# Kernel tuning notes

Hardware: AMD Instinct MI355X
Metric: run time of the kernel (lower is better)

Reference implementation:

```python
import jax, jax.numpy as jnp
import numpy as np

N_HEADS = 8
N_POINTS = 4


def _bilinear_sample(vl, g, Hl, Wl):
    # vl: [B, nH, Hl*Wl, hd] level values; g: [B, Q, nH, P, 2] sampling locs in [0,1] (x, y)
    # Emulates torch grid_sample(mode='bilinear', padding_mode='zeros', align_corners=False)
    B, Q, nH, P, _ = g.shape
    hd = vl.shape[-1]
    x = g[..., 0] * Wl - 0.5
    y = g[..., 1] * Hl - 0.5
    x0f = jnp.floor(x)
    y0f = jnp.floor(y)
    x0 = x0f.astype(jnp.int32)
    y0 = y0f.astype(jnp.int32)
    wx1 = x - x0f
    wy1 = y - y0f

    def corner(xi, yi, w):
        valid = (xi >= 0) & (xi < Wl) & (yi >= 0) & (yi < Hl)
        idx = jnp.clip(yi, 0, Hl - 1) * Wl + jnp.clip(xi, 0, Wl - 1)  # [B,Q,nH,P]
        idx = idx.transpose(0, 2, 1, 3).reshape(B, nH, Q * P)
        gathered = jnp.take_along_axis(vl, idx[..., None], axis=2)  # [B,nH,Q*P,hd]
        wm = (w * valid.astype(w.dtype)).transpose(0, 2, 1, 3).reshape(B, nH, Q * P)
        return gathered * wm[..., None]

    s = (corner(x0, y0, (1.0 - wx1) * (1.0 - wy1))
         + corner(x0 + 1, y0, wx1 * (1.0 - wy1))
         + corner(x0, y0 + 1, (1.0 - wx1) * wy1)
         + corner(x0 + 1, y0 + 1, wx1 * wy1))
    return s.reshape(B, nH, Q, P, hd)


def setup_inputs() -> dict:
    key = jax.random.key(0)
    ks = jax.random.split(key, 12)
    B, Q, D = 32, 300, 256
    L, P, nH = 4, N_POINTS, N_HEADS
    shapes = np.array([[80, 80], [40, 40], [20, 20], [10, 10]], dtype=np.int32)
    V = int((shapes[:, 0] * shapes[:, 1]).sum())  # 8500
    lsi = np.concatenate([[0], np.cumsum(shapes[:, 0] * shapes[:, 1])[:-1]]).astype(np.int32)
    sd = 1.0 / np.sqrt(D)
    return {
        'query': jax.random.normal(ks[0], (B, Q, D), jnp.float32),
        'reference_points': jax.random.uniform(ks[1], (B, Q, L, 2), jnp.float32),
        'value': jax.random.normal(ks[2], (B, V, D), jnp.float32),
        'spatial_shapes': jnp.asarray(shapes),
        'level_start_index': jnp.asarray(lsi),
        'W_off': jax.random.normal(ks[3], (D, nH * L * P * 2), jnp.float32) * sd,
        'b_off': jax.random.normal(ks[4], (nH * L * P * 2,), jnp.float32) * 0.5,
        'W_attn': jax.random.normal(ks[5], (D, nH * L * P), jnp.float32) * sd,
        'b_attn': jax.random.normal(ks[6], (nH * L * P,), jnp.float32) * 0.1,
        'W_val': jax.random.normal(ks[7], (D, D), jnp.float32) * sd,
        'b_val': jnp.zeros((D,), jnp.float32),
        'W_out': jax.random.normal(ks[8], (D, D), jnp.float32) * sd,
        'b_out': jnp.zeros((D,), jnp.float32),
    }


def reference(query, reference_points, value, spatial_shapes, level_start_index,
              W_off, b_off, W_attn, b_attn, W_val, b_val, W_out, b_out):
    shapes = np.asarray(spatial_shapes)  # static level shapes
    B, Q, D = query.shape
    nH, P = N_HEADS, N_POINTS
    L = shapes.shape[0]
    hd = D // nH

    val = value @ W_val + b_val  # [B,V,D]
    val = val.reshape(B, -1, nH, hd).transpose(0, 2, 1, 3)  # [B,nH,V,hd]

    off = (query @ W_off + b_off).reshape(B, Q, nH, L, P, 2)
    attn = jax.nn.softmax((query @ W_attn + b_attn).reshape(B, Q, nH, L * P), axis=-1)
    attn = attn.reshape(B, Q, nH, L, P)

    # normalizer is (W_l, H_l)
    norm = jnp.asarray(np.stack([shapes[:, 1], shapes[:, 0]], -1), jnp.float32)  # [L,2]
    loc = reference_points[:, :, None, :, None, :] + off / norm[None, None, None, :, None, :]

    out = jnp.zeros((B, Q, nH, hd), query.dtype)
    start = 0
    for lvl in range(L):
        Hl, Wl = int(shapes[lvl, 0]), int(shapes[lvl, 1])
        vl = val[:, :, start:start + Hl * Wl, :]  # [B,nH,HW,hd]
        sampled = _bilinear_sample(vl, loc[:, :, :, lvl], Hl, Wl)  # [B,nH,Q,P,hd]
        out = out + jnp.einsum('bnqpd,bqnp->bqnd', sampled, attn[:, :, :, lvl])
        start += Hl * Wl

    return out.reshape(B, Q, D) @ W_out + b_out
```

## Files before the change

### kernel.cpp

```cpp
#include <hip/hip_runtime.h>
#include <math.h>
#include <stdint.h>

#define NB 32
#define NQ 300
#define ND 256
#define NH 8
#define HD 32
#define NL 4
#define NP 4
#define V_TOT 8500
#define BQ_TOT (NB*NQ)
#define MVAL (NB*V_TOT)
#define NOA 384

typedef short v8s __attribute__((ext_vector_type(8)));
typedef float v4f __attribute__((ext_vector_type(4)));

#define AS1 __attribute__((address_space(1)))
#define AS3 __attribute__((address_space(3)))

__device__ __forceinline__ void copy16_async(const void* g, void* l) {
#if __has_builtin(__builtin_amdgcn_global_load_lds)
    __builtin_amdgcn_global_load_lds((const AS1 unsigned int*)g,
                                     (AS3 unsigned int*)l, 16, 0, 0);
#else
    *(uint4*)l = *(const uint4*)g;
#endif
}

__device__ __forceinline__ unsigned short f2bf_rne(float x) {
    unsigned u = __float_as_uint(x);
    u += 0x7fffu + ((u >> 16) & 1u);
    return (unsigned short)(u >> 16);
}
__device__ __forceinline__ float bf2f(unsigned short b) {
    return __uint_as_float(((unsigned)b) << 16);
}

__device__ __forceinline__ int swz_pos(int n, int k) {
    const int base = k & ~31;
    const int o = (k >> 3) & 3;
    const int op = o ^ ((n >> 1) & 3);
    return n * 256 + base + (op << 3) + (k & 7);
}

__global__ __launch_bounds__(256) void prep_weights(
    const float* __restrict__ W_val, const float* __restrict__ W_off,
    const float* __restrict__ W_attn, const float* __restrict__ W_out,
    const float* __restrict__ b_off, const float* __restrict__ b_attn,
    unsigned short* __restrict__ Bval_h, unsigned short* __restrict__ Bval_l,
    unsigned short* __restrict__ Boa_h,  unsigned short* __restrict__ Boa_l,
    unsigned short* __restrict__ Bout_h, unsigned short* __restrict__ Bout_l,
    float* __restrict__ b_oa)
{
    const int t = blockIdx.x * 256 + threadIdx.x;
    if (t < 65536) {
        const int n = t >> 8, k = t & 255;
        const float x = W_val[k * 256 + n];
        const unsigned short hi = f2bf_rne(x);
        const unsigned short lo = f2bf_rne(x - bf2f(hi));
        const int p = swz_pos(n, k);
        Bval_h[p] = hi; Bval_l[p] = lo;
    } else if (t < 65536 + 98304) {
        const int t2 = t - 65536;
        const int n = t2 >> 8, k = t2 & 255;
        const float x = (n < 256) ? W_off[k * 256 + n] : W_attn[k * 128 + (n - 256)];
        const unsigned short hi = f2bf_rne(x);
        const unsigned short lo = f2bf_rne(x - bf2f(hi));
        const int p = swz_pos(n, k);
        Boa_h[p] = hi; Boa_l[p] = lo;
    } else if (t < 229376) {
        const int t3 = t - 163840;
        const int n = t3 >> 8, k = t3 & 255;
        const float x = W_out[k * 256 + n];
        const unsigned short hi = f2bf_rne(x);
        const unsigned short lo = f2bf_rne(x - bf2f(hi));
        const int p = swz_pos(n, k);
        Bout_h[p] = hi; Bout_l[p] = lo;
    } else {
        const int t4 = t - 229376;
        if (t4 < NOA) b_oa[t4] = (t4 < 256) ? b_off[t4] : b_attn[t4 - 256];
    }
}

__global__ __launch_bounds__(256) void gemm_a32(
    const float* __restrict__ A,
    const unsigned short* __restrict__ Bh,
    const unsigned short* __restrict__ Bl,
    const float* __restrict__ bias,
    float* __restrict__ Cf,
    unsigned short* __restrict__ Cb,
    int ldc, int mode)
{
    __shared__ unsigned short Ah[128][40];
    __shared__ unsigned short Al[128][40];
    __shared__ unsigned short Bs[2][128][32];

    const int tid  = threadIdx.x;
    const int row0 = blockIdx.x * 128;
    const int col0 = blockIdx.y * 128;
    const int wave = tid >> 6;
    const int lane = tid & 63;
    const int wm   = (wave >> 1) * 64;
    const int wn   = (wave & 1) * 64;
    const int m16  = lane & 15;
    const int quad = lane >> 4;

    v4f acc[4][4] = {};

    for (int k0 = 0; k0 < 256; k0 += 32) {
        unsigned hpk[2][4], lpk[2][4];
        int rr[2], oo[2];
#pragma unroll
        for (int i = 0; i < 2; ++i) {
            const int idx = tid + i * 256;
            const int r   = idx >> 2;
            const int oct = (idx & 3) << 3;
            rr[i] = r; oo[i] = oct;
            const float4 f0 = *(const float4*)(A + (size_t)(row0 + r) * 256 + k0 + oct);
            const float4 f1 = *(const float4*)(A + (size_t)(row0 + r) * 256 + k0 + oct + 4);
            const float fe[8] = {f0.x, f0.y, f0.z, f0.w, f1.x, f1.y, f1.z, f1.w};
#pragma unroll
            for (int e = 0; e < 4; ++e) {
                const unsigned u0 = __float_as_uint(fe[2*e]);
                const unsigned u1 = __float_as_uint(fe[2*e+1]);
                hpk[i][e] = (u0 >> 16) | (u1 & 0xffff0000u);
                const float l0 = fe[2*e]   - __uint_as_float(u0 & 0xffff0000u);
                const float l1 = fe[2*e+1] - __uint_as_float(u1 & 0xffff0000u);
                lpk[i][e] = (__float_as_uint(l0) >> 16) | (__float_as_uint(l1) & 0xffff0000u);
            }
        }

        __syncthreads();

#pragma unroll
        for (int c = 0; c < 2; ++c) {
            const int linear = (wave * 2 + c) * 1024 + lane * 16;
            const int n   = linear >> 6;
            const int off = linear & 63;
            copy16_async((const char*)Bh + ((size_t)(col0 + n) * 256 + k0) * 2 + off,
                         (char*)&Bs[0][0][0] + linear);
            copy16_async((const char*)Bl + ((size_t)(col0 + n) * 256 + k0) * 2 + off,
                         (char*)&Bs[1][0][0] + linear);
        }

#pragma unroll
        for (int i = 0; i < 2; ++i) {
            *(uint4*)&Ah[rr[i]][oo[i]] = make_uint4(hpk[i][0], hpk[i][1], hpk[i][2], hpk[i][3]);
            *(uint4*)&Al[rr[i]][oo[i]] = make_uint4(lpk[i][0], lpk[i][1], lpk[i][2], lpk[i][3]);
        }

        __syncthreads();

        v8s ah[4], al[4], bh[4], bl[4];
#pragma unroll
        for (int i = 0; i < 4; ++i) {
            ah[i] = *(v8s*)&Ah[wm + i * 16 + m16][quad * 8];
            al[i] = *(v8s*)&Al[wm + i * 16 + m16][quad * 8];
            const int n  = wn + i * 16 + m16;
            const int ko = (quad ^ ((n >> 1) & 3)) << 3;
            bh[i] = *(v8s*)&Bs[0][n][ko];
            bl[i] = *(v8s*)&Bs[1][n][ko];
        }
#pragma unroll
        for (int i = 0; i < 4; ++i)
#pragma unroll
            for (int j = 0; j < 4; ++j) {
                acc[i][j] = __builtin_amdgcn_mfma_f32_16x16x32_bf16(ah[i], bh[j], acc[i][j], 0, 0, 0);
                acc[i][j] = __builtin_amdgcn_mfma_f32_16x16x32_bf16(ah[i], bl[j], acc[i][j], 0, 0, 0);
                acc[i][j] = __builtin_amdgcn_mfma_f32_16x16x32_bf16(al[i], bh[j], acc[i][j], 0, 0, 0);
            }
    }

#pragma unroll
    for (int j = 0; j < 4; ++j) {
        const int cl = col0 + wn + j * 16 + m16;
        const float bb = bias[cl];
        if (mode == 0) {
#pragma unroll
            for (int i = 0; i < 4; ++i)
#pragma unroll
                for (int r = 0; r < 4; ++r) {
                    const int R = row0 + wm + i * 16 + quad * 4 + r;
                    Cf[(size_t)R * ldc + cl] = acc[i][j][r] + bb;
                }
        } else {
            const int h  = cl >> 5;
            const int dh = cl & 31;
#pragma unroll
            for (int i = 0; i < 4; ++i)
#pragma unroll
                for (int r = 0; r < 4; ++r) {
                    const int R = row0 + wm + i * 16 + quad * 4 + r;
                    const unsigned b = (unsigned)R / V_TOT;
                    const int v = R - (int)b * V_TOT;
                    Cb[(((size_t)(b * NH + h)) * V_TOT + v) * HD + dh] =
                        f2bf_rne(acc[i][j][r] + bb);
                }
        }
    }
}

__global__ __launch_bounds__(256) void gemm_a16(
    const unsigned short* __restrict__ A,
    const unsigned short* __restrict__ Bh,
    const unsigned short* __restrict__ Bl,
    const float* __restrict__ bias,
    float* __restrict__ C, int ldc)
{
    __shared__ unsigned short As[128][32];
    __shared__ unsigned short Bs[2][128][32];

    const int tid  = threadIdx.x;
    const int row0 = blockIdx.x * 128;
    const int col0 = blockIdx.y * 128;
    const int wave = tid >> 6;
    const int lane = tid & 63;
    const int wm   = (wave >> 1) * 64;
    const int wn   = (wave & 1) * 64;
    const int m16  = lane & 15;
    const int quad = lane >> 4;

    v4f acc[4][4] = {};

    for (int k0 = 0; k0 < 256; k0 += 32) {
        __syncthreads();
#pragma unroll
        for (int c = 0; c < 2; ++c) {
            const int linear = (wave * 2 + c) * 1024 + lane * 16;
            const int n   = linear >> 6;
            const int off = linear & 63;
            copy16_async((const char*)A  + ((size_t)(row0 + n) * 256 + k0) * 2 + off,
                         (char*)&As[0][0] + linear);
            copy16_async((const char*)Bh + ((size_t)(col0 + n) * 256 + k0) * 2 + off,
                         (char*)&Bs[0][0][0] + linear);
            copy16_async((const char*)Bl + ((size_t)(col0 + n) * 256 + k0) * 2 + off,
                         (char*)&Bs[1][0][0] + linear);
        }
        __syncthreads();

        v8s a[4], bh[4], bl[4];
#pragma unroll
        for (int i = 0; i < 4; ++i) {
            const int r  = wm + i * 16 + m16;
            const int ka = (quad ^ ((r >> 1) & 3)) << 3;
            a[i] = *(v8s*)&As[r][ka];
            const int n  = wn + i * 16 + m16;
            const int kb = (quad ^ ((n >> 1) & 3)) << 3;
            bh[i] = *(v8s*)&Bs[0][n][kb];
            bl[i] = *(v8s*)&Bs[1][n][kb];
        }
#pragma unroll
        for (int i = 0; i < 4; ++i)
#pragma unroll
            for (int j = 0; j < 4; ++j) {
                acc[i][j] = __builtin_amdgcn_mfma_f32_16x16x32_bf16(a[i], bh[j], acc[i][j], 0, 0, 0);
                acc[i][j] = __builtin_amdgcn_mfma_f32_16x16x32_bf16(a[i], bl[j], acc[i][j], 0, 0, 0);
            }
    }

#pragma unroll
    for (int j = 0; j < 4; ++j) {
        const int cl = col0 + wn + j * 16 + m16;
        const float bb = bias[cl];
#pragma unroll
        for (int i = 0; i < 4; ++i)
#pragma unroll
            for (int r = 0; r < 4; ++r) {
                const int R = row0 + wm + i * 16 + quad * 4 + r;
                C[(size_t)R * ldc + cl] = acc[i][j][r] + bb;
            }
    }
}

__global__ __launch_bounds__(256) void sample_kernel(
    const float* __restrict__ refp,
    const float* __restrict__ offattn,
    const unsigned short* __restrict__ val,
    unsigned short* __restrict__ pre)
{
    const int t  = blockIdx.x * 256 + threadIdx.x;
    const int d8 = t & 3;
    const int h  = (t >> 2) & 7;
    const int bq = t >> 5;
    const int b  = bq / NQ;

    const float* rp = refp + (size_t)bq * 8;
    const float* op = offattn + (size_t)bq * 384 + h * 32;
    const float* ap = offattn + (size_t)bq * 384 + 256 + h * 16;

    float aw[16];
    float m = -1e30f;
#pragma unroll
    for (int i = 0; i < 16; ++i) { aw[i] = ap[i]; m = fmaxf(m, aw[i]); }
    float s = 0.f;
#pragma unroll
    for (int i = 0; i < 16; ++i) { aw[i] = __expf(aw[i] - m); s += aw[i]; }
    const float inv = 1.f / s;
#pragma unroll
    for (int i = 0; i < 16; ++i) aw[i] *= inv;

    const int Hs[4] = {80, 40, 20, 10};
    const int St[4] = {0, 6400, 8000, 8400};

    float acc[8] = {};
#pragma unroll
    for (int l = 0; l < NL; ++l) {
        const int Wl = Hs[l], Hl = Hs[l];
        const float fW = (float)Wl, fH = (float)Hl;
        const float rx = rp[l * 2 + 0];
        const float ry = rp[l * 2 + 1];
        const unsigned short* vb =
            val + (((size_t)(b * NH + h)) * V_TOT + St[l]) * HD + d8 * 8;
#pragma unroll
        for (int p = 0; p < NP; ++p) {
            const float ox = op[l * 8 + p * 2 + 0];
            const float oy = op[l * 8 + p * 2 + 1];
            const float w  = aw[l * 4 + p];
            const float x = fmaf(rx, fW, ox) - 0.5f;
            const float y = fmaf(ry, fH, oy) - 0.5f;
            const float x0f = floorf(x), y0f = floorf(y);
            const int   x0 = (int)x0f,  y0 = (int)y0f;
            const float wx1 = x - x0f,  wy1 = y - y0f;
            const float wx0 = 1.f - wx1, wy0 = 1.f - wy1;
#pragma unroll
            for (int cy = 0; cy < 2; ++cy) {
#pragma unroll
                for (int cx = 0; cx < 2; ++cx) {
                    const int xi = x0 + cx;
                    const int yi = y0 + cy;
                    float cw = (cx ? wx1 : wx0) * (cy ? wy1 : wy0) * w;
                    const bool valid = (xi >= 0) && (xi < Wl) && (yi >= 0) && (yi < Hl);
                    cw = valid ? cw : 0.f;
                    const int xc = xi < 0 ? 0 : (xi > Wl - 1 ? Wl - 1 : xi);
                    const int yc = yi < 0 ? 0 : (yi > Hl - 1 ? Hl - 1 : yi);
                    const uint4 g = *(const uint4*)(vb + (size_t)(yc * Wl + xc) * HD);
                    const unsigned gu[4] = {g.x, g.y, g.z, g.w};
#pragma unroll
                    for (int e = 0; e < 4; ++e) {
                        acc[2*e]   = fmaf(cw, __uint_as_float(gu[e] << 16),        acc[2*e]);
                        acc[2*e+1] = fmaf(cw, __uint_as_float(gu[e] & 0xffff0000u), acc[2*e+1]);
                    }
                }
            }
        }
    }

    unsigned o[4];
#pragma unroll
    for (int e = 0; e < 4; ++e)
        o[e] = (unsigned)f2bf_rne(acc[2*e]) | ((unsigned)f2bf_rne(acc[2*e+1]) << 16);
    const int octswz = d8 ^ ((bq >> 1) & 3);
    *(uint4*)(pre + (size_t)bq * 256 + h * 32 + octswz * 8) =
        make_uint4(o[0], o[1], o[2], o[3]);
}

extern "C" void kernel_launch(void* const* d_in, const int* in_sizes, int n_in,
                              void* d_out, int out_size, void* d_ws, size_t ws_size,
                              hipStream_t stream)
{
    const float* query  = (const float*)d_in[0];
    const float* refp   = (const float*)d_in[1];
    const float* value  = (const float*)d_in[2];
    const float* W_off  = (const float*)d_in[5];
    const float* b_off  = (const float*)d_in[6];
    const float* W_attn = (const float*)d_in[7];
    const float* b_attn = (const float*)d_in[8];
    const float* W_val  = (const float*)d_in[9];
    const float* b_val  = (const float*)d_in[10];
    const float* W_out  = (const float*)d_in[11];
    const float* b_out  = (const float*)d_in[12];
    float* out = (float*)d_out;

    char* ws = (char*)d_ws;
    unsigned short* val     = (unsigned short*)ws;
    float*          offattn = (float*)(ws + 139264000);
    unsigned short* pre     = (unsigned short*)(ws + 154009600);
    unsigned short* Bval_h  = (unsigned short*)(ws + 158924800);
    unsigned short* Bval_l  = Bval_h + 65536;
    unsigned short* Boa_h   = Bval_l + 65536;
    unsigned short* Boa_l   = Boa_h + 98304;
    unsigned short* Bout_h  = Boa_l + 98304;
    unsigned short* Bout_l  = Bout_h + 65536;
    float*          b_oa    = (float*)(Bout_l + 65536);

    const dim3 blk(256);

    prep_weights<<<dim3(898), blk, 0, stream>>>(
        W_val, W_off, W_attn, W_out, b_off, b_attn,
        Bval_h, Bval_l, Boa_h, Boa_l, Bout_h, Bout_l, b_oa);

    gemm_a32<<<dim3(MVAL / 128, 2), blk, 0, stream>>>(
        value, Bval_h, Bval_l, b_val, nullptr, val, 0, 1);

    gemm_a32<<<dim3(BQ_TOT / 128, 3), blk, 0, stream>>>(
        query, Boa_h, Boa_l, b_oa, offattn, nullptr, NOA, 0);

    sample_kernel<<<dim3((BQ_TOT * 32) / 256), blk, 0, stream>>>(
        refp, offattn, val, pre);

    gemm_a16<<<dim3(BQ_TOT / 128, 2), blk, 0, stream>>>(
        pre, Bout_h, Bout_l, b_out, out, 256);
}
```

Baseline: 618.4 us.

## Double-buffer LDS tiles in both GEMM kernels to overlap loads with MFMA

Both the fp32-A and bf16-A GEMM kernels now keep two LDS buffers for the A and B tiles. The next K-slice's global loads (async LDS copies for B, register prefetch plus bf16 hi/lo split for A) are issued before the current slice's MFMAs, leaving one barrier per iteration instead of two. The aim is to hide global memory latency behind the MFMA work. In exchange, LDS use per block roughly doubles, which may reduce occupancy, and the A-prefetch registers raise register pressure.

```diff
diff --git a/kernel.cpp b/kernel.cpp
--- a/kernel.cpp
+++ b/kernel.cpp
@@ -93,9 +93,9 @@
     unsigned short* __restrict__ Cb,
     int ldc, int mode)
 {
-    __shared__ unsigned short Ah[128][40];
-    __shared__ unsigned short Al[128][40];
-    __shared__ unsigned short Bs[2][128][32];
+    __shared__ unsigned short Ah[2][128][40];
+    __shared__ unsigned short Al[2][128][40];
+    __shared__ unsigned short Bs[2][2][128][32];
 
     const int tid  = threadIdx.x;
     const int row0 = blockIdx.x * 128;
@@ -107,62 +107,88 @@
     const int m16  = lane & 15;
     const int quad = lane >> 4;
 
+    int rr[2], oo[2];
+#pragma unroll
+    for (int i = 0; i < 2; ++i) {
+        const int idx = tid + i * 256;
+        rr[i] = idx >> 2;
+        oo[i] = (idx & 3) << 3;
+    }
+
     v4f acc[4][4] = {};
-
-    for (int k0 = 0; k0 < 256; k0 += 32) {
-        unsigned hpk[2][4], lpk[2][4];
-        int rr[2], oo[2];
-#pragma unroll
-        for (int i = 0; i < 2; ++i) {
-            const int idx = tid + i * 256;
-            const int r   = idx >> 2;
-            const int oct = (idx & 3) << 3;
-            rr[i] = r; oo[i] = oct;
-            const float4 f0 = *(const float4*)(A + (size_t)(row0 + r) * 256 + k0 + oct);
-            const float4 f1 = *(const float4*)(A + (size_t)(row0 + r) * 256 + k0 + oct + 4);
-            const float fe[8] = {f0.x, f0.y, f0.z, f0.w, f1.x, f1.y, f1.z, f1.w};
-#pragma unroll
-            for (int e = 0; e < 4; ++e) {
-                const unsigned u0 = __float_as_uint(fe[2*e]);
-                const unsigned u1 = __float_as_uint(fe[2*e+1]);
-                hpk[i][e] = (u0 >> 16) | (u1 & 0xffff0000u);
-                const float l0 = fe[2*e]   - __uint_as_float(u0 & 0xffff0000u);
-                const float l1 = fe[2*e+1] - __uint_as_float(u1 & 0xffff0000u);
-                lpk[i][e] = (__float_as_uint(l0) >> 16) | (__float_as_uint(l1) & 0xffff0000u);
-            }
-        }
-
-        __syncthreads();
-
-#pragma unroll
-        for (int c = 0; c < 2; ++c) {
-            const int linear = (wave * 2 + c) * 1024 + lane * 16;
-            const int n   = linear >> 6;
-            const int off = linear & 63;
-            copy16_async((const char*)Bh + ((size_t)(col0 + n) * 256 + k0) * 2 + off,
-                         (char*)&Bs[0][0][0] + linear);
-            copy16_async((const char*)Bl + ((size_t)(col0 + n) * 256 + k0) * 2 + off,
-                         (char*)&Bs[1][0][0] + linear);
-        }
-
-#pragma unroll
-        for (int i = 0; i < 2; ++i) {
-            *(uint4*)&Ah[rr[i]][oo[i]] = make_uint4(hpk[i][0], hpk[i][1], hpk[i][2], hpk[i][3]);
-            *(uint4*)&Al[rr[i]][oo[i]] = make_uint4(lpk[i][0], lpk[i][1], lpk[i][2], lpk[i][3]);
-        }
-
-        __syncthreads();
+    float fe[2][8];
+
+#pragma unroll
+    for (int c = 0; c < 2; ++c) {
+        const int linear = (wave * 2 + c) * 1024 + lane * 16;
+        const int n   = linear >> 6;
+        const int off = linear & 63;
+        copy16_async((const char*)Bh + ((size_t)(col0 + n) * 256 + 0) * 2 + off,
+                     (char*)&Bs[0][0][0][0] + linear);
+        copy16_async((const char*)Bl + ((size_t)(col0 + n) * 256 + 0) * 2 + off,
+                     (char*)&Bs[0][1][0][0] + linear);
+    }
+#pragma unroll
+    for (int i = 0; i < 2; ++i) {
+        const float4 f0 = *(const float4*)(A + (size_t)(row0 + rr[i]) * 256 + oo[i]);
+        const float4 f1 = *(const float4*)(A + (size_t)(row0 + rr[i]) * 256 + oo[i] + 4);
+        fe[i][0] = f0.x; fe[i][1] = f0.y; fe[i][2] = f0.z; fe[i][3] = f0.w;
+        fe[i][4] = f1.x; fe[i][5] = f1.y; fe[i][6] = f1.z; fe[i][7] = f1.w;
+    }
+#pragma unroll
+    for (int i = 0; i < 2; ++i) {
+        unsigned hpk[4], lpk[4];
+#pragma unroll
+        for (int e = 0; e < 4; ++e) {
+            const unsigned u0 = __float_as_uint(fe[i][2*e]);
+            const unsigned u1 = __float_as_uint(fe[i][2*e+1]);
+            hpk[e] = (u0 >> 16) | (u1 & 0xffff0000u);
+            const float l0 = fe[i][2*e]   - __uint_as_float(u0 & 0xffff0000u);
+            const float l1 = fe[i][2*e+1] - __uint_as_float(u1 & 0xffff0000u);
+            lpk[e] = (__float_as_uint(l0) >> 16) | (__float_as_uint(l1) & 0xffff0000u);
+        }
+        *(uint4*)&Ah[0][rr[i]][oo[i]] = make_uint4(hpk[0], hpk[1], hpk[2], hpk[3]);
+        *(uint4*)&Al[0][rr[i]][oo[i]] = make_uint4(lpk[0], lpk[1], lpk[2], lpk[3]);
+    }
+
+    __syncthreads();
+
+    for (int t = 0; t < 8; ++t) {
+        const int buf = t & 1;
+        const int nb  = buf ^ 1;
+        const int k1  = (t + 1) << 5;
+
+        if (t < 7) {
+#pragma unroll
+            for (int i = 0; i < 2; ++i) {
+                const float4 f0 = *(const float4*)(A + (size_t)(row0 + rr[i]) * 256 + k1 + oo[i]);
+                const float4 f1 = *(const float4*)(A + (size_t)(row0 + rr[i]) * 256 + k1 + oo[i] + 4);
+                fe[i][0] = f0.x; fe[i][1] = f0.y; fe[i][2] = f0.z; fe[i][3] = f0.w;
+                fe[i][4] = f1.x; fe[i][5] = f1.y; fe[i][6] = f1.z; fe[i][7] = f1.w;
+            }
+#pragma unroll
+            for (int c = 0; c < 2; ++c) {
+                const int linear = (wave * 2 + c) * 1024 + lane * 16;
+                const int n   = linear >> 6;
+                const int off = linear & 63;
+                copy16_async((const char*)Bh + ((size_t)(col0 + n) * 256 + k1) * 2 + off,
+                             (char*)&Bs[nb][0][0][0] + linear);
+                copy16_async((const char*)Bl + ((size_t)(col0 + n) * 256 + k1) * 2 + off,
+                             (char*)&Bs[nb][1][0][0] + linear);
+            }
+        }
 
         v8s ah[4], al[4], bh[4], bl[4];
 #pragma unroll
         for (int i = 0; i < 4; ++i) {
-            ah[i] = *(v8s*)&Ah[wm + i * 16 + m16][quad * 8];
-            al[i] = *(v8s*)&Al[wm + i * 16 + m16][quad * 8];
+            ah[i] = *(v8s*)&Ah[buf][wm + i * 16 + m16][quad * 8];
+            al[i] = *(v8s*)&Al[buf][wm + i * 16 + m16][quad * 8];
             const int n  = wn + i * 16 + m16;
             const int ko = (quad ^ ((n >> 1) & 3)) << 3;
-            bh[i] = *(v8s*)&Bs[0][n][ko];
-            bl[i] = *(v8s*)&Bs[1][n][ko];
-        }
+            bh[i] = *(v8s*)&Bs[buf][0][n][ko];
+            bl[i] = *(v8s*)&Bs[buf][1][n][ko];
+        }
+
 #pragma unroll
         for (int i = 0; i < 4; ++i)
 #pragma unroll
@@ -171,6 +197,26 @@
                 acc[i][j] = __builtin_amdgcn_mfma_f32_16x16x32_bf16(ah[i], bl[j], acc[i][j], 0, 0, 0);
                 acc[i][j] = __builtin_amdgcn_mfma_f32_16x16x32_bf16(al[i], bh[j], acc[i][j], 0, 0, 0);
             }
+
+        if (t < 7) {
+#pragma unroll
+            for (int i = 0; i < 2; ++i) {
+                unsigned hpk[4], lpk[4];
+#pragma unroll
+                for (int e = 0; e < 4; ++e) {
+                    const unsigned u0 = __float_as_uint(fe[i][2*e]);
+                    const unsigned u1 = __float_as_uint(fe[i][2*e+1]);
+                    hpk[e] = (u0 >> 16) | (u1 & 0xffff0000u);
+                    const float l0 = fe[i][2*e]   - __uint_as_float(u0 & 0xffff0000u);
+                    const float l1 = fe[i][2*e+1] - __uint_as_float(u1 & 0xffff0000u);
+                    lpk[e] = (__float_as_uint(l0) >> 16) | (__float_as_uint(l1) & 0xffff0000u);
+                }
+                *(uint4*)&Ah[nb][rr[i]][oo[i]] = make_uint4(hpk[0], hpk[1], hpk[2], hpk[3]);
+                *(uint4*)&Al[nb][rr[i]][oo[i]] = make_uint4(lpk[0], lpk[1], lpk[2], lpk[3]);
+            }
+        }
+
+        __syncthreads();
     }
 
 #pragma unroll
@@ -209,8 +255,8 @@
     const float* __restrict__ bias,
     float* __restrict__ C, int ldc)
 {
-    __shared__ unsigned short As[128][32];
-    __shared__ unsigned short Bs[2][128][32];
+    __shared__ unsigned short As[2][128][32];
+    __shared__ unsigned short Bs[2][2][128][32];
 
     const int tid  = threadIdx.x;
     const int row0 = blockIdx.x * 128;
@@ -224,32 +270,50 @@
 
     v4f acc[4][4] = {};
 
-    for (int k0 = 0; k0 < 256; k0 += 32) {
-        __syncthreads();
-#pragma unroll
-        for (int c = 0; c < 2; ++c) {
-            const int linear = (wave * 2 + c) * 1024 + lane * 16;
-            const int n   = linear >> 6;
-            const int off = linear & 63;
-            copy16_async((const char*)A  + ((size_t)(row0 + n) * 256 + k0) * 2 + off,
-                         (char*)&As[0][0] + linear);
-            copy16_async((const char*)Bh + ((size_t)(col0 + n) * 256 + k0) * 2 + off,
-                         (char*)&Bs[0][0][0] + linear);
-            copy16_async((const char*)Bl + ((size_t)(col0 + n) * 256 + k0) * 2 + off,
-                         (char*)&Bs[1][0][0] + linear);
-        }
-        __syncthreads();
+#pragma unroll
+    for (int c = 0; c < 2; ++c) {
+        const int linear = (wave * 2 + c) * 1024 + lane * 16;
+        const int n   = linear >> 6;
+        const int off = linear & 63;
+        copy16_async((const char*)A  + ((size_t)(row0 + n) * 256 + 0) * 2 + off,
+                     (char*)&As[0][0][0] + linear);
+        copy16_async((const char*)Bh + ((size_t)(col0 + n) * 256 + 0) * 2 + off,
+                     (char*)&Bs[0][0][0][0] + linear);
+        copy16_async((const char*)Bl + ((size_t)(col0 + n) * 256 + 0) * 2 + off,
+                     (char*)&Bs[0][1][0][0] + linear);
+    }
+    __syncthreads();
+
+    for (int t = 0; t < 8; ++t) {
+        const int buf = t & 1;
+        const int nb  = buf ^ 1;
+        const int k1  = (t + 1) << 5;
+
+        if (t < 7) {
+#pragma unroll
+            for (int c = 0; c < 2; ++c) {
+                const int linear = (wave * 2 + c) * 1024 + lane * 16;
+                const int n   = linear >> 6;
+                const int off = linear & 63;
+                copy16_async((const char*)A  + ((size_t)(row0 + n) * 256 + k1) * 2 + off,
+                             (char*)&As[nb][0][0] + linear);
+                copy16_async((const char*)Bh + ((size_t)(col0 + n) * 256 + k1) * 2 + off,
+                             (char*)&Bs[nb][0][0][0] + linear);
+                copy16_async((const char*)Bl + ((size_t)(col0 + n) * 256 + k1) * 2 + off,
+                             (char*)&Bs[nb][1][0][0] + linear);
+            }
+        }
 
         v8s a[4], bh[4], bl[4];
 #pragma unroll
         for (int i = 0; i < 4; ++i) {
             const int r  = wm + i * 16 + m16;
             const int ka = (quad ^ ((r >> 1) & 3)) << 3;
-            a[i] = *(v8s*)&As[r][ka];
+            a[i] = *(v8s*)&As[buf][r][ka];
             const int n  = wn + i * 16 + m16;
             const int kb = (quad ^ ((n >> 1) & 3)) << 3;
-            bh[i] = *(v8s*)&Bs[0][n][kb];
-            bl[i] = *(v8s*)&Bs[1][n][kb];
+            bh[i] = *(v8s*)&Bs[buf][0][n][kb];
+            bl[i] = *(v8s*)&Bs[buf][1][n][kb];
         }
 #pragma unroll
         for (int i = 0; i < 4; ++i)
@@ -258,6 +322,8 @@
                 acc[i][j] = __builtin_amdgcn_mfma_f32_16x16x32_bf16(a[i], bh[j], acc[i][j], 0, 0, 0);
                 acc[i][j] = __builtin_amdgcn_mfma_f32_16x16x32_bf16(a[i], bl[j], acc[i][j], 0, 0, 0);
             }
+
+        __syncthreads();
     }
 
 #pragma unroll
```

Result: no change. 629.0 us (+1.7%).

## Double-buffer gemm_a16 LDS loads, swizzle gemm_a32 A tile, use packed bf16 split

Applied to the files above, without the earlier changes.

gemm_a16 now double-buffers its LDS tiles. The next k-slice's async global-to-LDS copies are issued before the MFMAs on the current slice, which removes one barrier per iteration and overlaps loads with compute. gemm_a32 replaces its padded A tiles with an XOR-swizzled layout to avoid LDS bank conflicts. It also splits fp32 into hi/lo bf16 with packed round-to-nearest conversions instead of truncation. The double buffer doubles LDS use in gemm_a16, which may lower occupancy, and the rounding change slightly alters the numerics of the split.

```diff
diff --git a/kernel.cpp b/kernel.cpp
--- a/kernel.cpp
+++ b/kernel.cpp
@@ -1,4 +1,5 @@
 #include <hip/hip_runtime.h>
+#include <hip/hip_bf16.h>
 #include <math.h>
 #include <stdint.h>
 
@@ -36,6 +37,19 @@
 }
 __device__ __forceinline__ float bf2f(unsigned short b) {
     return __uint_as_float(((unsigned)b) << 16);
+}
+
+__device__ __forceinline__ void split2(float f0, float f1,
+                                       unsigned& hp, unsigned& lp) {
+    float2 v; v.x = f0; v.y = f1;
+    __hip_bfloat162 h = __float22bfloat162_rn(v);
+    unsigned hu; __builtin_memcpy(&hu, &h, 4);
+    const float h0 = __uint_as_float(hu << 16);
+    const float h1 = __uint_as_float(hu & 0xffff0000u);
+    float2 l; l.x = f0 - h0; l.y = f1 - h1;
+    __hip_bfloat162 lo = __float22bfloat162_rn(l);
+    unsigned lu; __builtin_memcpy(&lu, &lo, 4);
+    hp = hu; lp = lu;
 }
 
 __device__ __forceinline__ int swz_pos(int n, int k) {
@@ -93,8 +107,8 @@
     unsigned short* __restrict__ Cb,
     int ldc, int mode)
 {
-    __shared__ unsigned short Ah[128][40];
-    __shared__ unsigned short Al[128][40];
+    __shared__ unsigned short Ah[128][32];
+    __shared__ unsigned short Al[128][32];
     __shared__ unsigned short Bs[2][128][32];
 
     const int tid  = threadIdx.x;
@@ -116,20 +130,15 @@
         for (int i = 0; i < 2; ++i) {
             const int idx = tid + i * 256;
             const int r   = idx >> 2;
-            const int oct = (idx & 3) << 3;
-            rr[i] = r; oo[i] = oct;
-            const float4 f0 = *(const float4*)(A + (size_t)(row0 + r) * 256 + k0 + oct);
-            const float4 f1 = *(const float4*)(A + (size_t)(row0 + r) * 256 + k0 + oct + 4);
-            const float fe[8] = {f0.x, f0.y, f0.z, f0.w, f1.x, f1.y, f1.z, f1.w};
-#pragma unroll
-            for (int e = 0; e < 4; ++e) {
-                const unsigned u0 = __float_as_uint(fe[2*e]);
-                const unsigned u1 = __float_as_uint(fe[2*e+1]);
-                hpk[i][e] = (u0 >> 16) | (u1 & 0xffff0000u);
-                const float l0 = fe[2*e]   - __uint_as_float(u0 & 0xffff0000u);
-                const float l1 = fe[2*e+1] - __uint_as_float(u1 & 0xffff0000u);
-                lpk[i][e] = (__float_as_uint(l0) >> 16) | (__float_as_uint(l1) & 0xffff0000u);
-            }
+            const int o   = idx & 3;
+            rr[i] = r;
+            oo[i] = (o ^ ((r >> 1) & 3)) << 3;
+            const float4 f0 = *(const float4*)(A + (size_t)(row0 + r) * 256 + k0 + o * 8);
+            const float4 f1 = *(const float4*)(A + (size_t)(row0 + r) * 256 + k0 + o * 8 + 4);
+            split2(f0.x, f0.y, hpk[i][0], lpk[i][0]);
+            split2(f0.z, f0.w, hpk[i][1], lpk[i][1]);
+            split2(f1.x, f1.y, hpk[i][2], lpk[i][2]);
+            split2(f1.z, f1.w, hpk[i][3], lpk[i][3]);
         }
 
         __syncthreads();
@@ -156,8 +165,10 @@
         v8s ah[4], al[4], bh[4], bl[4];
 #pragma unroll
         for (int i = 0; i < 4; ++i) {
-            ah[i] = *(v8s*)&Ah[wm + i * 16 + m16][quad * 8];
-            al[i] = *(v8s*)&Al[wm + i * 16 + m16][quad * 8];
+            const int r  = wm + i * 16 + m16;
+            const int ka = (quad ^ ((r >> 1) & 3)) << 3;
+            ah[i] = *(v8s*)&Ah[r][ka];
+            al[i] = *(v8s*)&Al[r][ka];
             const int n  = wn + i * 16 + m16;
             const int ko = (quad ^ ((n >> 1) & 3)) << 3;
             bh[i] = *(v8s*)&Bs[0][n][ko];
@@ -209,8 +220,8 @@
     const float* __restrict__ bias,
     float* __restrict__ C, int ldc)
 {
-    __shared__ unsigned short As[128][32];
-    __shared__ unsigned short Bs[2][128][32];
+    __shared__ unsigned short As[2][128][32];
+    __shared__ unsigned short Bs[2][2][128][32];
 
     const int tid  = threadIdx.x;
     const int row0 = blockIdx.x * 128;
@@ -224,32 +235,50 @@
 
     v4f acc[4][4] = {};
 
-    for (int k0 = 0; k0 < 256; k0 += 32) {
-        __syncthreads();
-#pragma unroll
-        for (int c = 0; c < 2; ++c) {
-            const int linear = (wave * 2 + c) * 1024 + lane * 16;
-            const int n   = linear >> 6;
-            const int off = linear & 63;
-            copy16_async((const char*)A  + ((size_t)(row0 + n) * 256 + k0) * 2 + off,
-                         (char*)&As[0][0] + linear);
-            copy16_async((const char*)Bh + ((size_t)(col0 + n) * 256 + k0) * 2 + off,
-                         (char*)&Bs[0][0][0] + linear);
-            copy16_async((const char*)Bl + ((size_t)(col0 + n) * 256 + k0) * 2 + off,
-                         (char*)&Bs[1][0][0] + linear);
-        }
-        __syncthreads();
+#pragma unroll
+    for (int c = 0; c < 2; ++c) {
+        const int linear = (wave * 2 + c) * 1024 + lane * 16;
+        const int n   = linear >> 6;
+        const int off = linear & 63;
+        copy16_async((const char*)A  + ((size_t)(row0 + n) * 256 + 0) * 2 + off,
+                     (char*)&As[0][0][0] + linear);
+        copy16_async((const char*)Bh + ((size_t)(col0 + n) * 256 + 0) * 2 + off,
+                     (char*)&Bs[0][0][0][0] + linear);
+        copy16_async((const char*)Bl + ((size_t)(col0 + n) * 256 + 0) * 2 + off,
+                     (char*)&Bs[0][1][0][0] + linear);
+    }
+    __syncthreads();
+
+    for (int t = 0; t < 8; ++t) {
+        const int buf = t & 1;
+        const int nb  = buf ^ 1;
+        const int k1  = (t + 1) << 5;
+
+        if (t < 7) {
+#pragma unroll
+            for (int c = 0; c < 2; ++c) {
+                const int linear = (wave * 2 + c) * 1024 + lane * 16;
+                const int n   = linear >> 6;
+                const int off = linear & 63;
+                copy16_async((const char*)A  + ((size_t)(row0 + n) * 256 + k1) * 2 + off,
+                             (char*)&As[nb][0][0] + linear);
+                copy16_async((const char*)Bh + ((size_t)(col0 + n) * 256 + k1) * 2 + off,
+                             (char*)&Bs[nb][0][0][0] + linear);
+                copy16_async((const char*)Bl + ((size_t)(col0 + n) * 256 + k1) * 2 + off,
+                             (char*)&Bs[nb][1][0][0] + linear);
+            }
+        }
 
         v8s a[4], bh[4], bl[4];
 #pragma unroll
         for (int i = 0; i < 4; ++i) {
             const int r  = wm + i * 16 + m16;
             const int ka = (quad ^ ((r >> 1) & 3)) << 3;
-            a[i] = *(v8s*)&As[r][ka];
+            a[i] = *(v8s*)&As[buf][r][ka];
             const int n  = wn + i * 16 + m16;
             const int kb = (quad ^ ((n >> 1) & 3)) << 3;
-            bh[i] = *(v8s*)&Bs[0][n][kb];
-            bl[i] = *(v8s*)&Bs[1][n][kb];
+            bh[i] = *(v8s*)&Bs[buf][0][n][kb];
+            bl[i] = *(v8s*)&Bs[buf][1][n][kb];
         }
 #pragma unroll
         for (int i = 0; i < 4; ++i)
@@ -258,6 +287,8 @@
                 acc[i][j] = __builtin_amdgcn_mfma_f32_16x16x32_bf16(a[i], bh[j], acc[i][j], 0, 0, 0);
                 acc[i][j] = __builtin_amdgcn_mfma_f32_16x16x32_bf16(a[i], bl[j], acc[i][j], 0, 0, 0);
             }
+
+        __syncthreads();
     }
 
 #pragma unroll
```

Result: no change. 617.2 us (-0.2%).
